# Performance work log

Measured on AMD Instinct MI355X. Metric: run time of the kernel, lower is better.

The kernel has to match this reference:

```python
import jax, jax.numpy as jnp
import numpy as np

B, S, D = 4, 2048, 1024
H, DH = 16, 64
SCALE = 1.0 / np.sqrt(DH).astype(np.float32)


def setup_inputs() -> dict:
    key = jax.random.key(0)
    ks = jax.random.split(key, 12)
    s = 0.02
    inp = {
        "Q": jax.random.normal(ks[0], (B, S, D), jnp.float32),
        "K": jax.random.normal(ks[1], (B, S, D), jnp.float32),
        "V": jax.random.normal(ks[2], (B, S, D), jnp.float32),
        # True = masked position; causal mask broadcast over batch
        "attention_mask": jnp.broadcast_to(
            jnp.triu(jnp.ones((S, S), jnp.bool_), k=1), (B, S, S)
        ),
        "wq": jax.random.normal(ks[3], (D, H * DH), jnp.float32) * s,
        "bq": jnp.zeros((H * DH,), jnp.float32),
        "wk": jax.random.normal(ks[4], (D, H * DH), jnp.float32) * s,
        "bk": jnp.zeros((H * DH,), jnp.float32),
        "wv": jax.random.normal(ks[5], (D, H * DH), jnp.float32) * s,
        "bv": jnp.zeros((H * DH,), jnp.float32),
        "wo": jax.random.normal(ks[6], (H * DH, D), jnp.float32) * s,
        "bo": jnp.zeros((D,), jnp.float32),
    }
    return inp


def reference(Q, K, V, attention_mask, wq, bq, wk, bk, wv, bv, wo, bo):
    b = Q.shape[0]
    # project and split heads: [b, H, S, DH]
    q = (Q @ wq + bq).reshape(b, -1, H, DH).transpose(0, 2, 1, 3)
    k = (K @ wk + bk).reshape(b, -1, H, DH).transpose(0, 2, 1, 3)
    v = (V @ wv + bv).reshape(b, -1, H, DH).transpose(0, 2, 1, 3)
    # scores: [b, H, Sq, Sk]
    scores = jnp.einsum("bhqd,bhkd->bhqk", q, k) * SCALE
    scores = jnp.where(attention_mask[:, None, :, :], -1e9, scores)
    attn = jax.nn.softmax(scores, axis=-1)
    # dropout is identity at inference
    ctx = jnp.einsum("bhqk,bhkd->bhqd", attn, v)
    ctx = ctx.transpose(0, 2, 1, 3).reshape(b, -1, H * DH)
    out = ctx @ wo + bo
    return out, attn
```

## Files before the change

kernel.cpp:

```cpp
#include <hip/hip_runtime.h>
#include <hip/hip_bf16.h>

typedef __bf16 bf16_t;
typedef __bf16 bf16x8 __attribute__((ext_vector_type(8)));
typedef float f32x4 __attribute__((ext_vector_type(4)));
typedef unsigned short u16x8 __attribute__((ext_vector_type(8)));

#define B_ 4
#define S_ 2048
#define D_ 1024
#define H_ 16
#define DH_ 64
#define SCALE_ 0.125f
#define NEGBIG_ (-30000.0f)
#define OUTOFF_ ((size_t)B_ * S_ * D_)
#define PROJ_ ((size_t)B_ * S_ * H_ * DH_)

__global__ void detect_kernel(const unsigned* __restrict__ q, int* __restrict__ flag)
{
  __shared__ int cnt;
  if (threadIdx.x == 0) cnt = 0;
  __syncthreads();
  int local = 0;
  for (int i = threadIdx.x; i < 256; i += 64) {
    unsigned lo = q[i] & 0xFFFFu;
    unsigned e = (lo >> 7) & 0xFFu;
    if (e >= 110u && e <= 130u) local++;
  }
  atomicAdd(&cnt, local);
  __syncthreads();
  if (threadIdx.x == 0) *flag = (cnt >= 96) ? 1 : 0;
}

__global__ __launch_bounds__(256) void transpose_w_kernel(
    const void* __restrict__ W, bf16_t* __restrict__ WT,
    const int* __restrict__ flagp)
{
  __shared__ bf16_t T[64 * 72];
  const int flag = *flagp;
  const int tid = threadIdx.x;
  const int k0 = blockIdx.x * 64, n0 = blockIdx.y * 64;
  const int r = tid >> 3, c = (tid & 7) * 8;

#pragma unroll
  for (int it = 0; it < 2; ++it) {
    int kr = r + it * 32;
    bf16x8 v;
    if (flag) {
      v = *(const bf16x8*)((const bf16_t*)W + (size_t)(k0 + kr) * 1024 + n0 + c);
    } else {
      const float* Wf = (const float*)W + (size_t)(k0 + kr) * 1024 + n0 + c;
      f32x4 x0 = *(const f32x4*)Wf;
      f32x4 x1 = *(const f32x4*)(Wf + 4);
#pragma unroll
      for (int j = 0; j < 4; j++) { v[j] = (bf16_t)x0[j]; v[4 + j] = (bf16_t)x1[j]; }
    }
#pragma unroll
    for (int j = 0; j < 8; j++) T[(c + j) * 72 + kr] = v[j];
  }
  __syncthreads();
#pragma unroll
  for (int it = 0; it < 2; ++it) {
    int nr = r + it * 32;
    bf16x8 v = *(const bf16x8*)&T[nr * 72 + c];
    *(bf16x8*)(WT + (size_t)(n0 + nr) * 1024 + k0 + c) = v;
  }
}

__global__ __launch_bounds__(256) void gemm128_kernel(
    const void* __restrict__ A, const bf16_t* __restrict__ BT,
    const void* __restrict__ bias, void* __restrict__ out,
    int headsplit, int a_follows_flag, const int* __restrict__ flagp)
{
  __shared__ bf16_t As[128 * 72];
  __shared__ bf16_t Bs[128 * 72];
  const int flag = *flagp;
  const bool a_bf = a_follows_flag ? (flag == 1) : true;
  const int tid = threadIdx.x;
  const int wave = tid >> 6, lane = tid & 63;
  const int quad = lane >> 4, l15 = lane & 15;
  const int wm = wave >> 1, wn = wave & 1;
  const int n0 = blockIdx.x * 128, m0 = blockIdx.y * 128;
  const int srow = tid >> 3, scol = (tid & 7) * 8;

  f32x4 acc[4][4];
#pragma unroll
  for (int m = 0; m < 4; m++)
#pragma unroll
    for (int n = 0; n < 4; n++) acc[m][n] = (f32x4){0.f, 0.f, 0.f, 0.f};

  for (int k0 = 0; k0 < 1024; k0 += 64) {
#pragma unroll
    for (int it = 0; it < 4; ++it) {
      int row = srow + it * 32;
      size_t gidx = (size_t)(m0 + row) * 1024 + k0 + scol;
      bf16x8 av;
      if (a_bf) {
        av = *(const bf16x8*)((const bf16_t*)A + gidx);
      } else {
        const float* Af = (const float*)A + gidx;
        f32x4 x0 = *(const f32x4*)Af;
        f32x4 x1 = *(const f32x4*)(Af + 4);
#pragma unroll
        for (int j = 0; j < 4; j++) { av[j] = (bf16_t)x0[j]; av[4 + j] = (bf16_t)x1[j]; }
      }
      *(bf16x8*)&As[row * 72 + scol] = av;
      *(bf16x8*)&Bs[row * 72 + scol] =
          *(const bf16x8*)(BT + (size_t)(n0 + row) * 1024 + k0 + scol);
    }
    __syncthreads();

#pragma unroll
    for (int kc = 0; kc < 2; ++kc) {
      bf16x8 fa[4], fb[4];
#pragma unroll
      for (int m = 0; m < 4; m++)
        fa[m] = *(const bf16x8*)&As[(wm * 64 + m * 16 + l15) * 72 + kc * 32 + quad * 8];
#pragma unroll
      for (int n = 0; n < 4; n++)
        fb[n] = *(const bf16x8*)&Bs[(wn * 64 + n * 16 + l15) * 72 + kc * 32 + quad * 8];
#pragma unroll
      for (int m = 0; m < 4; m++)
#pragma unroll
        for (int n = 0; n < 4; n++)
          acc[m][n] = __builtin_amdgcn_mfma_f32_16x16x32_bf16(fa[m], fb[n], acc[m][n], 0, 0, 0);
    }
    __syncthreads();
  }

#pragma unroll
  for (int n = 0; n < 4; n++) {
    int col = n0 + wn * 64 + n * 16 + l15;
    float bvv = flag ? (float)((const bf16_t*)bias)[col] : ((const float*)bias)[col];
#pragma unroll
    for (int m = 0; m < 4; m++) {
#pragma unroll
      for (int r = 0; r < 4; r++) {
        int row = m0 + wm * 64 + m * 16 + quad * 4 + r;
        float v = acc[m][n][r] + bvv;
        if (headsplit) {
          int b = row >> 11, s = row & 2047;
          int h = col >> 6, d = col & 63;
          ((bf16_t*)out)[(((size_t)(b * H_ + h)) * S_ + s) * DH_ + d] = (bf16_t)v;
        } else if (flag) {
          ((bf16_t*)out)[(size_t)row * 1024 + col] = (bf16_t)v;
        } else {
          ((float*)out)[(size_t)row * 1024 + col] = v;
        }
      }
    }
  }
}

__global__ __launch_bounds__(256) void attn_kernel(
    const bf16_t* __restrict__ q, const bf16_t* __restrict__ k,
    const bf16_t* __restrict__ v, void* __restrict__ d_out_raw,
    bf16_t* __restrict__ ctx, const int* __restrict__ flagp)
{
  const int flag = *flagp;
  const int qt = blockIdx.x;
  const int bh = blockIdx.y;
  const bf16_t* qb = q + (size_t)bh * S_ * DH_;
  const bf16_t* kb = k + (size_t)bh * S_ * DH_;
  const bf16_t* vb = v + (size_t)bh * S_ * DH_;
  bf16_t* attn_b16 = (bf16_t*)d_out_raw + OUTOFF_ + (size_t)bh * S_ * S_;
  float*  attn_f32 = (float*)d_out_raw + OUTOFF_ + (size_t)bh * S_ * S_;

  __shared__ bf16_t Ks[64 * 72];
  __shared__ bf16_t Vt[64 * 72];
  __shared__ bf16_t Ps[64 * 72];
  __shared__ float sm_m[64], sm_l[64];

  const int tid = threadIdx.x;
  const int wave = tid >> 6, lane = tid & 63;
  const int quad = lane >> 4, l15 = lane & 15;

  const bf16_t* qrow = qb + (size_t)(qt * 64 + wave * 16 + l15) * DH_;
  bf16x8 aq0 = *(const bf16x8*)&qrow[quad * 8];
  bf16x8 aq1 = *(const bf16x8*)&qrow[32 + quad * 8];

  float m_run[4], l_run[4];
#pragma unroll
  for (int r = 0; r < 4; r++) { m_run[r] = NEGBIG_; l_run[r] = 0.f; }

  for (int kt = 0; kt <= qt; ++kt) {
    for (int c = tid; c < 512; c += 256) {
      int row = c >> 3, off = (c & 7) * 8;
      *(bf16x8*)&Ks[row * 72 + off] =
          *(const bf16x8*)&kb[(size_t)(kt * 64 + row) * DH_ + off];
    }
    __syncthreads();

    float sc[4][4];
#pragma unroll
    for (int nb = 0; nb < 4; nb++) {
      f32x4 c = (f32x4){0.f, 0.f, 0.f, 0.f};
      bf16x8 b0 = *(const bf16x8*)&Ks[(nb * 16 + l15) * 72 + quad * 8];
      c = __builtin_amdgcn_mfma_f32_16x16x32_bf16(aq0, b0, c, 0, 0, 0);
      bf16x8 b1 = *(const bf16x8*)&Ks[(nb * 16 + l15) * 72 + 32 + quad * 8];
      c = __builtin_amdgcn_mfma_f32_16x16x32_bf16(aq1, b1, c, 0, 0, 0);
      int kcol = kt * 64 + nb * 16 + l15;
#pragma unroll
      for (int r = 0; r < 4; r++) {
        int qrow_g = qt * 64 + wave * 16 + quad * 4 + r;
        float s = c[r] * SCALE_;
        if (kcol > qrow_g) s = NEGBIG_;
        sc[nb][r] = s;
      }
    }
#pragma unroll
    for (int r = 0; r < 4; r++) {
      float tmax = fmaxf(fmaxf(sc[0][r], sc[1][r]), fmaxf(sc[2][r], sc[3][r]));
#pragma unroll
      for (int off = 8; off >= 1; off >>= 1) tmax = fmaxf(tmax, __shfl_xor(tmax, off));
      float nm = fmaxf(m_run[r], tmax);
      float ps = 0.f;
#pragma unroll
      for (int nb = 0; nb < 4; nb++) ps += __expf(sc[nb][r] - nm);
#pragma unroll
      for (int off = 8; off >= 1; off >>= 1) ps += __shfl_xor(ps, off);
      l_run[r] = l_run[r] * __expf(m_run[r] - nm) + ps;
      m_run[r] = nm;
    }
    __syncthreads();
  }

  if (l15 == 0) {
#pragma unroll
    for (int r = 0; r < 4; r++) {
      sm_m[wave * 16 + quad * 4 + r] = m_run[r];
      sm_l[wave * 16 + quad * 4 + r] = l_run[r];
    }
  }
  __syncthreads();

  f32x4 acc[4];
#pragma unroll
  for (int nb = 0; nb < 4; nb++) acc[nb] = (f32x4){0.f, 0.f, 0.f, 0.f};

  for (int kt = 0; kt <= qt; ++kt) {
    for (int c = tid; c < 512; c += 256) {
      int row = c >> 3, off = (c & 7) * 8;
      *(bf16x8*)&Ks[row * 72 + off] =
          *(const bf16x8*)&kb[(size_t)(kt * 64 + row) * DH_ + off];
      bf16x8 vv = *(const bf16x8*)&vb[(size_t)(kt * 64 + row) * DH_ + off];
#pragma unroll
      for (int i = 0; i < 8; i++) Vt[(off + i) * 72 + row] = vv[i];
    }
    __syncthreads();

#pragma unroll
    for (int nb = 0; nb < 4; nb++) {
      f32x4 c = (f32x4){0.f, 0.f, 0.f, 0.f};
      bf16x8 b0 = *(const bf16x8*)&Ks[(nb * 16 + l15) * 72 + quad * 8];
      c = __builtin_amdgcn_mfma_f32_16x16x32_bf16(aq0, b0, c, 0, 0, 0);
      bf16x8 b1 = *(const bf16x8*)&Ks[(nb * 16 + l15) * 72 + 32 + quad * 8];
      c = __builtin_amdgcn_mfma_f32_16x16x32_bf16(aq1, b1, c, 0, 0, 0);
      int kcol = kt * 64 + nb * 16 + l15;
#pragma unroll
      for (int r = 0; r < 4; r++) {
        int qloc = wave * 16 + quad * 4 + r;
        int qrow_g = qt * 64 + qloc;
        float s = c[r] * SCALE_;
        if (kcol > qrow_g) s = NEGBIG_;
        float p = __expf(s - sm_m[qloc]) / sm_l[qloc];
        Ps[qloc * 72 + nb * 16 + l15] = (bf16_t)p;
      }
    }
    __syncthreads();

#pragma unroll
    for (int ks = 0; ks < 2; ks++) {
      bf16x8 ap = *(const bf16x8*)&Ps[(wave * 16 + l15) * 72 + ks * 32 + quad * 8];
#pragma unroll
      for (int nb = 0; nb < 4; nb++) {
        bf16x8 bv_ = *(const bf16x8*)&Vt[(nb * 16 + l15) * 72 + ks * 32 + quad * 8];
        acc[nb] = __builtin_amdgcn_mfma_f32_16x16x32_bf16(ap, bv_, acc[nb], 0, 0, 0);
      }
    }
    for (int c = tid; c < 512; c += 256) {
      int row = c >> 3, off = (c & 7) * 8;
      size_t gidx = (size_t)(qt * 64 + row) * S_ + kt * 64 + off;
      if (flag) {
        *(u16x8*)&attn_b16[gidx] = *(const u16x8*)&Ps[row * 72 + off];
      } else {
        f32x4 a0, a1;
#pragma unroll
        for (int i = 0; i < 4; i++) {
          a0[i] = (float)Ps[row * 72 + off + i];
          a1[i] = (float)Ps[row * 72 + off + 4 + i];
        }
        *(f32x4*)&attn_f32[gidx] = a0;
        *(f32x4*)&attn_f32[gidx + 4] = a1;
      }
    }
    __syncthreads();
  }

  for (int kt = qt + 1; kt < 32; ++kt) {
    for (int c = tid; c < 512; c += 256) {
      int row = c >> 3, off = (c & 7) * 8;
      size_t gidx = (size_t)(qt * 64 + row) * S_ + kt * 64 + off;
      if (flag) {
        *(u16x8*)&attn_b16[gidx] = (u16x8){0, 0, 0, 0, 0, 0, 0, 0};
      } else {
        *(f32x4*)&attn_f32[gidx] = (f32x4){0.f, 0.f, 0.f, 0.f};
        *(f32x4*)&attn_f32[gidx + 4] = (f32x4){0.f, 0.f, 0.f, 0.f};
      }
    }
  }

  int b = bh >> 4, h = bh & 15;
#pragma unroll
  for (int nb = 0; nb < 4; nb++) {
    int d = nb * 16 + l15;
#pragma unroll
    for (int r = 0; r < 4; r++) {
      int query = qt * 64 + wave * 16 + quad * 4 + r;
      ctx[((size_t)(b * S_ + query)) * (H_ * DH_) + h * DH_ + d] = (bf16_t)acc[nb][r];
    }
  }
}

extern "C" void kernel_launch(void* const* d_in, const int* in_sizes, int n_in,
                              void* d_out, int out_size, void* d_ws, size_t ws_size,
                              hipStream_t stream)
{
  const void* Q  = d_in[0];
  const void* K  = d_in[1];
  const void* V  = d_in[2];
  const void* wq = d_in[4];
  const void* bq = d_in[5];
  const void* wk = d_in[6];
  const void* bk = d_in[7];
  const void* wv = d_in[8];
  const void* bv = d_in[9];
  const void* wo = d_in[10];
  const void* bo = d_in[11];

  int* flag = (int*)d_ws;
  bf16_t* qws = (bf16_t*)((char*)d_ws + 16);
  bf16_t* kws = qws + PROJ_;
  bf16_t* vws = kws + PROJ_;
  bf16_t* cws = vws + PROJ_;
  bf16_t* wT_pre  = cws;
  bf16_t* wT_post = qws;

  detect_kernel<<<1, 64, 0, stream>>>((const unsigned*)Q, flag);

  dim3 tg(16, 16);
  dim3 gg(8, 64);

  transpose_w_kernel<<<tg, 256, 0, stream>>>(wq, wT_pre, flag);
  gemm128_kernel<<<gg, 256, 0, stream>>>(Q, wT_pre, bq, qws, 1, 1, flag);

  transpose_w_kernel<<<tg, 256, 0, stream>>>(wk, wT_pre, flag);
  gemm128_kernel<<<gg, 256, 0, stream>>>(K, wT_pre, bk, kws, 1, 1, flag);

  transpose_w_kernel<<<tg, 256, 0, stream>>>(wv, wT_pre, flag);
  gemm128_kernel<<<gg, 256, 0, stream>>>(V, wT_pre, bv, vws, 1, 1, flag);

  attn_kernel<<<dim3(32, 64), 256, 0, stream>>>(qws, kws, vws, d_out, cws, flag);

  transpose_w_kernel<<<tg, 256, 0, stream>>>(wo, wT_post, flag);
  gemm128_kernel<<<gg, 256, 0, stream>>>(cws, wT_post, bo, d_out, 0, 0, flag);
}
```

Baseline: 1.824 ms.

## Register-prefetch next K/V tiles and XOR-swizzle transposed V in shared memory

Measured after the change: 1.718 ms. 5.8% less time.

```diff
diff --git a/kernel.cpp b/kernel.cpp
--- a/kernel.cpp
+++ b/kernel.cpp
@@ -152,6 +152,8 @@
   }
 }
 
+#define VT_PHYS(d, key) ((d) * 72 + ((((key) >> 3) ^ ((d) >> 3)) & 7) * 8 + ((key) & 7))
+
 __global__ __launch_bounds__(256) void attn_kernel(
     const bf16_t* __restrict__ q, const bf16_t* __restrict__ k,
     const bf16_t* __restrict__ v, void* __restrict__ d_out_raw,
@@ -174,6 +176,8 @@
   const int tid = threadIdx.x;
   const int wave = tid >> 6, lane = tid & 63;
   const int quad = lane >> 4, l15 = lane & 15;
+  const int r0 = tid >> 3, r1 = r0 + 32;
+  const int soff = (tid & 7) * 8;
 
   const bf16_t* qrow = qb + (size_t)(qt * 64 + wave * 16 + l15) * DH_;
   bf16x8 aq0 = *(const bf16x8*)&qrow[quad * 8];
@@ -183,12 +187,15 @@
 #pragma unroll
   for (int r = 0; r < 4; r++) { m_run[r] = NEGBIG_; l_run[r] = 0.f; }
 
+  bf16x8 ck0 = *(const bf16x8*)&kb[(size_t)r0 * DH_ + soff];
+  bf16x8 ck1 = *(const bf16x8*)&kb[(size_t)r1 * DH_ + soff];
+
   for (int kt = 0; kt <= qt; ++kt) {
-    for (int c = tid; c < 512; c += 256) {
-      int row = c >> 3, off = (c & 7) * 8;
-      *(bf16x8*)&Ks[row * 72 + off] =
-          *(const bf16x8*)&kb[(size_t)(kt * 64 + row) * DH_ + off];
-    }
+    *(bf16x8*)&Ks[r0 * 72 + soff] = ck0;
+    *(bf16x8*)&Ks[r1 * 72 + soff] = ck1;
+    int ktn = (kt + 1 <= qt) ? kt + 1 : qt;
+    bf16x8 nk0 = *(const bf16x8*)&kb[(size_t)(ktn * 64 + r0) * DH_ + soff];
+    bf16x8 nk1 = *(const bf16x8*)&kb[(size_t)(ktn * 64 + r1) * DH_ + soff];
     __syncthreads();
 
     float sc[4][4];
@@ -223,6 +230,7 @@
       m_run[r] = nm;
     }
     __syncthreads();
+    ck0 = nk0; ck1 = nk1;
   }
 
   if (l15 == 0) {
@@ -238,15 +246,24 @@
 #pragma unroll
   for (int nb = 0; nb < 4; nb++) acc[nb] = (f32x4){0.f, 0.f, 0.f, 0.f};
 
+  ck0 = *(const bf16x8*)&kb[(size_t)r0 * DH_ + soff];
+  ck1 = *(const bf16x8*)&kb[(size_t)r1 * DH_ + soff];
+  bf16x8 cv0 = *(const bf16x8*)&vb[(size_t)r0 * DH_ + soff];
+  bf16x8 cv1 = *(const bf16x8*)&vb[(size_t)r1 * DH_ + soff];
+
   for (int kt = 0; kt <= qt; ++kt) {
-    for (int c = tid; c < 512; c += 256) {
-      int row = c >> 3, off = (c & 7) * 8;
-      *(bf16x8*)&Ks[row * 72 + off] =
-          *(const bf16x8*)&kb[(size_t)(kt * 64 + row) * DH_ + off];
-      bf16x8 vv = *(const bf16x8*)&vb[(size_t)(kt * 64 + row) * DH_ + off];
-#pragma unroll
-      for (int i = 0; i < 8; i++) Vt[(off + i) * 72 + row] = vv[i];
-    }
+    *(bf16x8*)&Ks[r0 * 72 + soff] = ck0;
+    *(bf16x8*)&Ks[r1 * 72 + soff] = ck1;
+#pragma unroll
+    for (int i = 0; i < 8; i++) {
+      Vt[VT_PHYS(soff + i, r0)] = cv0[i];
+      Vt[VT_PHYS(soff + i, r1)] = cv1[i];
+    }
+    int ktn = (kt + 1 <= qt) ? kt + 1 : qt;
+    bf16x8 nk0 = *(const bf16x8*)&kb[(size_t)(ktn * 64 + r0) * DH_ + soff];
+    bf16x8 nk1 = *(const bf16x8*)&kb[(size_t)(ktn * 64 + r1) * DH_ + soff];
+    bf16x8 nv0 = *(const bf16x8*)&vb[(size_t)(ktn * 64 + r0) * DH_ + soff];
+    bf16x8 nv1 = *(const bf16x8*)&vb[(size_t)(ktn * 64 + r1) * DH_ + soff];
     __syncthreads();
 
 #pragma unroll
@@ -274,7 +291,9 @@
       bf16x8 ap = *(const bf16x8*)&Ps[(wave * 16 + l15) * 72 + ks * 32 + quad * 8];
 #pragma unroll
       for (int nb = 0; nb < 4; nb++) {
-        bf16x8 bv_ = *(const bf16x8*)&Vt[(nb * 16 + l15) * 72 + ks * 32 + quad * 8];
+        int d = nb * 16 + l15;
+        int swz = ((ks * 4 + quad) ^ ((d >> 3) & 7)) * 8;
+        bf16x8 bv_ = *(const bf16x8*)&Vt[d * 72 + swz];
         acc[nb] = __builtin_amdgcn_mfma_f32_16x16x32_bf16(ap, bv_, acc[nb], 0, 0, 0);
       }
     }
@@ -295,6 +314,7 @@
       }
     }
     __syncthreads();
+    ck0 = nk0; ck1 = nk1; cv0 = nv0; cv1 = nv1;
   }
 
   for (int kt = qt + 1; kt < 32; ++kt) {
```
